# Kernel tuning notes

Hardware: AMD Instinct MI355X
Metric: run time of the kernel (lower is better)

Reference implementation:

```python
import jax, jax.numpy as jnp
import numpy as np

N = 50000        # nodes
E = 1_600_000    # edges (avg degree 32)
G = 512          # graphs
F_IN = 9         # node features
H = 64           # hidden dim
ED = 1           # edge feature dim


def _lin(k, fo, fi):
    w = jax.random.normal(k, (fo, fi), jnp.float32) * (1.0 / np.sqrt(fi))
    b = jnp.zeros((fo,), jnp.float32)
    return w, b


def setup_inputs() -> dict:
    key = jax.random.key(0)
    ks = jax.random.split(key, 16)
    x = jax.random.normal(ks[0], (N, F_IN), jnp.float32)
    edge_index = jax.random.randint(ks[1], (2, E), 0, N, dtype=jnp.int64)
    edge_attr = jax.random.normal(ks[2], (E, ED), jnp.float32)
    batch = jnp.sort(jax.random.randint(ks[3], (N,), 0, G, dtype=jnp.int64))
    B_total = jax.random.uniform(ks[4], (G,), jnp.float32) * 100.0
    terminal_mask = jax.random.randint(ks[5], (N,), 0, 2, dtype=jnp.int32)
    c_cost = jax.random.uniform(ks[6], (N,), jnp.float32)
    # conv1: edge lin (ED->F_IN), nn = Linear(F_IN,H), Linear(H,H)
    e1_w, e1_b = _lin(ks[7], F_IN, ED)
    w1a, b1a = _lin(ks[8], H, F_IN)
    w1b, b1b = _lin(ks[9], H, H)
    # conv2: edge lin (ED->H), nn = Linear(H,H), Linear(H,H)
    e2_w, e2_b = _lin(ks[10], H, ED)
    w2a, b2a = _lin(ks[11], H, H)
    w2b, b2b = _lin(ks[12], H, H)
    # readout: Linear(H,H//2), Linear(H//2,1)
    wr1, br1 = _lin(ks[13], H // 2, H)
    wr2, br2 = _lin(ks[14], 1, H // 2)
    return dict(x=x, edge_index=edge_index, edge_attr=edge_attr, batch=batch,
                B_total=B_total, terminal_mask=terminal_mask, c_cost=c_cost,
                e1_w=e1_w, e1_b=e1_b, w1a=w1a, b1a=b1a, w1b=w1b, b1b=b1b,
                e2_w=e2_w, e2_b=e2_b, w2a=w2a, b2a=b2a, w2b=w2b, b2b=b2b,
                wr1=wr1, br1=br1, wr2=wr2, br2=br2)


def _gine(x, src, dst, edge_attr, ew, eb, wa, ba, wb, bb):
    # GINEConv (eps=0): nn(x + sum_j relu(x_j + W_e e_ji))
    e = edge_attr @ ew.T + eb                    # [E, F]
    m = jax.nn.relu(x[src] + e)                  # [E, F] gather + edge fuse
    aggr = jax.ops.segment_sum(m, dst, num_segments=N)  # scatter-add -> [N, F]
    h = x + aggr
    h = jax.nn.relu(h @ wa.T + ba)
    h = jax.nn.relu(h @ wb.T + bb)
    return h


def reference(x, edge_index, edge_attr, batch, B_total, terminal_mask, c_cost,
              e1_w, e1_b, w1a, b1a, w1b, b1b,
              e2_w, e2_b, w2a, b2a, w2b, b2b,
              wr1, br1, wr2, br2):
    src, dst = edge_index[0], edge_index[1]
    h = _gine(x, src, dst, edge_attr, e1_w, e1_b, w1a, b1a, w1b, b1b)
    h = _gine(h, src, dst, edge_attr, e2_w, e2_b, w2a, b2a, w2b, b2b)
    pi_raw = jax.nn.sigmoid((jax.nn.relu(h @ wr1.T + br1) @ wr2.T + br2))[:, 0]
    pi_raw = pi_raw * (1.0 - terminal_mask.astype(jnp.float32))
    node_expenses = pi_raw * c_cost
    total_expenses = jax.ops.segment_sum(node_expenses, batch, num_segments=G)
    ratio = jnp.minimum(B_total[batch] / (total_expenses[batch] + 1e-12), 1.0)
    return pi_raw * ratio
```

## Files before the change

### kernel.cpp

```cpp
#include <hip/hip_runtime.h>
#include <hip/hip_fp16.h>
#include <math.h>

#define N_NODES 50000
#define N_EDGES 1600000
#define N_GRAPHS 512
#define F_IN 9
#define H 64
#define N_BUCKETS ((N_NODES + 255) >> 8)
#define EPB 4096
#define N_SBLK ((N_EDGES + EPB - 1) / EPB)
#define FINE_CAP 10240

typedef _Float16 f16x8 __attribute__((ext_vector_type(8)));
typedef float f32x4 __attribute__((ext_vector_type(4)));

__device__ __forceinline__ void pack_weights_body(
        const float* __restrict__ w1a, const float* __restrict__ w1b,
        const float* __restrict__ w2a, const float* __restrict__ w2b,
        const float* __restrict__ wr1,
        __half* __restrict__ pk1Ah, __half* __restrict__ pk1Al,
        __half* __restrict__ pk1Bh, __half* __restrict__ pk1Bl,
        __half* __restrict__ pkAh, __half* __restrict__ pkAl,
        __half* __restrict__ pkBh, __half* __restrict__ pkBl,
        __half* __restrict__ pkRh, __half* __restrict__ pkRl) {
    int t = threadIdx.x;
    for (int i = t; i < 2048; i += 512) {
        int j = i & 7, l = (i >> 3) & 63, tt = i >> 9;
        int q = l >> 4, n = l & 15;
        int k = q * 8 + j;
        float v = (k < F_IN) ? w1a[(tt * 16 + n) * F_IN + k] : 0.f;
        __half h = __float2half(v);
        pk1Ah[i] = h; pk1Al[i] = __float2half(v - __half2float(h));
    }
    for (int i = t; i < 4096; i += 512) {
        int j = i & 7, l = (i >> 3) & 63, c = (i >> 9) & 1, tt = i >> 10;
        int q = l >> 4, n = l & 15;
        int src = (tt * 16 + n) * H + c * 32 + q * 8 + j;
        float v1 = w1b[src], wa = w2a[src], wb = w2b[src];
        __half h1 = __float2half(v1), ah = __float2half(wa), bh = __float2half(wb);
        pk1Bh[i] = h1; pk1Bl[i] = __float2half(v1 - __half2float(h1));
        pkAh[i] = ah; pkAl[i] = __float2half(wa - __half2float(ah));
        pkBh[i] = bh; pkBl[i] = __float2half(wb - __half2float(bh));
    }
    for (int i = t; i < 2048; i += 512) {
        int j = i & 7, l = (i >> 3) & 63, c = (i >> 9) & 1, tt = i >> 10;
        int q = l >> 4, n = l & 15;
        float wr = wr1[(tt * 16 + n) * H + c * 32 + q * 8 + j];
        __half rh = __float2half(wr);
        pkRh[i] = rh; pkRl[i] = __float2half(wr - __half2float(rh));
    }
}

__global__ void __launch_bounds__(512)
bucket_scatter(const int* __restrict__ ei,
               const float* __restrict__ ea,
               int* __restrict__ bnext,
               uint2* __restrict__ ebuk,
               const float* __restrict__ w1a,
               const float* __restrict__ w1b,
               const float* __restrict__ w2a,
               const float* __restrict__ w2b,
               const float* __restrict__ wr1,
               __half* pk1Ah, __half* pk1Al,
               __half* pk1Bh, __half* pk1Bl,
               __half* pkAh, __half* pkAl,
               __half* pkBh, __half* pkBl,
               __half* pkRh, __half* pkRl) {
    if (blockIdx.x == 0) {
        pack_weights_body(w1a, w1b, w2a, w2b, wr1, pk1Ah, pk1Al, pk1Bh, pk1Bl,
                          pkAh, pkAl, pkBh, pkBl, pkRh, pkRl);
        return;
    }
    __shared__ int cnt[N_BUCKETS];
    __shared__ int gbase[N_BUCKETS];
    for (int i = threadIdx.x; i < N_BUCKETS; i += 512) cnt[i] = 0;
    __syncthreads();
    int base = (blockIdx.x - 1) * EPB;
    int rk[8];
#pragma unroll
    for (int j = 0; j < 8; ++j) {
        int e = base + j * 512 + threadIdx.x;
        rk[j] = -1;
        if (e < N_EDGES) {
            int d = ei[N_EDGES + e];
            int b = d >> 8;
            int r = atomicAdd(&cnt[b], 1);
            rk[j] = (b << 21) | ((d & 255) << 13) | r;
        }
    }
    __syncthreads();
    for (int i = threadIdx.x; i < N_BUCKETS; i += 512)
        gbase[i] = cnt[i] ? atomicAdd(&bnext[i], cnt[i]) : 0;
    __syncthreads();
#pragma unroll
    for (int j = 0; j < 8; ++j) {
        if (rk[j] < 0) continue;
        int e = base + j * 512 + threadIdx.x;
        int b = rk[j] >> 21, dl = (rk[j] >> 13) & 255, r = rk[j] & 8191;
        int slot = gbase[b] + r;
        if (slot >= FINE_CAP) continue;
        unsigned pay = ((unsigned)ei[e] << 16) |
                       (unsigned)__half_as_ushort(__float2half(ea[e]));
        ebuk[(size_t)b * FINE_CAP + slot] = make_uint2(pay, (unsigned)dl);
    }
}

__global__ void __launch_bounds__(512)
bucket_fine(const uint2* __restrict__ ebuk,
            const int* __restrict__ bnext,
            unsigned* __restrict__ ep4,
            int* __restrict__ starts, int* __restrict__ deg) {
    __shared__ unsigned sorted[FINE_CAP];
    __shared__ int cntN[256], offN[256], nxtN[256];
    __shared__ int wsum[4];
    int b = blockIdx.x;
    int base = b * FINE_CAP;
    int count = bnext[b];
    if (count > FINE_CAP) count = FINE_CAP;
    int tid = threadIdx.x;
    if (tid < 256) cntN[tid] = 0;
    __syncthreads();
    for (int i = tid; i < count; i += 512)
        atomicAdd(&cntN[ebuk[base + i].y], 1);
    __syncthreads();
    int lane = tid & 63, wid = tid >> 6;
    int v = 0, incl = 0;
    if (tid < 256) {
        v = cntN[tid]; incl = v;
#pragma unroll
        for (int off = 1; off < 64; off <<= 1) {
            int t = __shfl_up(incl, off, 64);
            if (lane >= off) incl += t;
        }
        if (lane == 63) wsum[wid] = incl;
    }
    __syncthreads();
    if (tid < 256) {
        int woff = 0;
        for (int w = 0; w < wid; ++w) woff += wsum[w];
        int excl = woff + incl - v;
        offN[tid] = excl;
        nxtN[tid] = 0;
        int n = (b << 8) + tid;
        if (n < N_NODES) { starts[n] = base + excl; deg[n] = v; }
    }
    __syncthreads();
    for (int i = tid; i < count; i += 512) {
        uint2 e = ebuk[base + i];
        int r = atomicAdd(&nxtN[e.y], 1);
        sorted[offN[e.y] + r] = e.x;
    }
    __syncthreads();
    for (int i = tid; i < count; i += 512)
        ep4[base + i] = sorted[i];
}

#define UNPACK_ATTR(P) __half2float(__ushort_as_half((unsigned short)((P) & 0xffffu)))

__global__ void agg1_kernel(const float* __restrict__ x,
                            const int* __restrict__ starts,
                            const int* __restrict__ deg,
                            const unsigned* __restrict__ ep4,
                            const float* __restrict__ e1w,
                            const float* __restrict__ e1b,
                            float* __restrict__ xs) {
    int n = blockIdx.x * (blockDim.x >> 6) + (threadIdx.x >> 6);
    int lane = threadIdx.x & 63;
    if (n >= N_NODES) return;
    int slot = lane >> 4;
    int f = lane & 15;
    int s0 = starts[n], dg = deg[n];
    bool act = f < F_IN;
    float wf = act ? e1w[f] : 0.f;
    float bf = act ? e1b[f] : 0.f;
    float acc = 0.f;
    int j = slot;
    for (; j + 12 < dg; j += 16) {
        unsigned pa = ep4[s0 + j];
        unsigned pb = ep4[s0 + j + 4];
        unsigned pc = ep4[s0 + j + 8];
        unsigned pd = ep4[s0 + j + 12];
        float xa_ = act ? x[(pa >> 16) * F_IN + f] : 0.f;
        float xb_ = act ? x[(pb >> 16) * F_IN + f] : 0.f;
        float xc_ = act ? x[(pc >> 16) * F_IN + f] : 0.f;
        float xd_ = act ? x[(pd >> 16) * F_IN + f] : 0.f;
        if (act) {
            acc += fmaxf(xa_ + UNPACK_ATTR(pa) * wf + bf, 0.f)
                 + fmaxf(xb_ + UNPACK_ATTR(pb) * wf + bf, 0.f)
                 + fmaxf(xc_ + UNPACK_ATTR(pc) * wf + bf, 0.f)
                 + fmaxf(xd_ + UNPACK_ATTR(pd) * wf + bf, 0.f);
        }
    }
    for (; j < dg; j += 4) {
        unsigned p = ep4[s0 + j];
        float xv = act ? x[(p >> 16) * F_IN + f] : 0.f;
        float m = xv + UNPACK_ATTR(p) * wf + bf;
        acc += act ? fmaxf(m, 0.f) : 0.f;
    }
    acc += __shfl_xor(acc, 16, 64);
    acc += __shfl_xor(acc, 32, 64);
    if (lane < 32)
        xs[n * 32 + lane] = (lane < F_IN) ? x[n * F_IN + lane] + acc : 0.f;
}

__device__ __forceinline__ void split8(const float* __restrict__ v,
                                       f16x8& hi, f16x8& lo) {
#pragma unroll
    for (int j = 0; j < 8; ++j) {
        _Float16 h = (_Float16)v[j];
        hi[j] = h;
        lo[j] = (_Float16)(v[j] - (float)h);
    }
}

#define TILE3(C, A0H, A0L, A1H, A1L, PH, PL, T) do {                          \
        f16x8 b0h = *(const f16x8*)((PH) + (((T) * 2 + 0) * 64 + lane) * 8);  \
        f16x8 b0l = *(const f16x8*)((PL) + (((T) * 2 + 0) * 64 + lane) * 8);  \
        f16x8 b1h = *(const f16x8*)((PH) + (((T) * 2 + 1) * 64 + lane) * 8);  \
        f16x8 b1l = *(const f16x8*)((PL) + (((T) * 2 + 1) * 64 + lane) * 8);  \
        C = __builtin_amdgcn_mfma_f32_16x16x32_f16(A0H, b0h, C, 0, 0, 0);     \
        C = __builtin_amdgcn_mfma_f32_16x16x32_f16(A0L, b0h, C, 0, 0, 0);     \
        C = __builtin_amdgcn_mfma_f32_16x16x32_f16(A0H, b0l, C, 0, 0, 0);     \
        C = __builtin_amdgcn_mfma_f32_16x16x32_f16(A1H, b1h, C, 0, 0, 0);     \
        C = __builtin_amdgcn_mfma_f32_16x16x32_f16(A1L, b1h, C, 0, 0, 0);     \
        C = __builtin_amdgcn_mfma_f32_16x16x32_f16(A1H, b1l, C, 0, 0, 0);     \
    } while (0)

__global__ void node1_kernel(const float* __restrict__ xs,
                             const __half* __restrict__ pk1Ah, const __half* __restrict__ pk1Al,
                             const float* __restrict__ b1a,
                             const __half* __restrict__ pk1Bh, const __half* __restrict__ pk1Bl,
                             const float* __restrict__ b1b,
                             __half* __restrict__ h1) {
    __shared__ float hbuf[4][16][68];
    int wv = threadIdx.x >> 6;
    int lane = threadIdx.x & 63;
    int gwave = blockIdx.x * 4 + wv;
    bool active = gwave < (N_NODES / 16);
    int base = active ? gwave * 16 : 0;
    int m = lane & 15, q = lane >> 4;
    const _Float16* pAh = (const _Float16*)pk1Ah;
    const _Float16* pAl = (const _Float16*)pk1Al;
    const _Float16* pBh = (const _Float16*)pk1Bh;
    const _Float16* pBl = (const _Float16*)pk1Bl;

    f16x8 ah, al;
    split8(xs + (size_t)(base + m) * 32 + q * 8, ah, al);
#pragma unroll
    for (int t = 0; t < 4; ++t) {
        f32x4 c = {0.f, 0.f, 0.f, 0.f};
        f16x8 bh = *(const f16x8*)(pAh + (t * 64 + lane) * 8);
        f16x8 bl = *(const f16x8*)(pAl + (t * 64 + lane) * 8);
        c = __builtin_amdgcn_mfma_f32_16x16x32_f16(ah, bh, c, 0, 0, 0);
        c = __builtin_amdgcn_mfma_f32_16x16x32_f16(al, bh, c, 0, 0, 0);
        c = __builtin_amdgcn_mfma_f32_16x16x32_f16(ah, bl, c, 0, 0, 0);
        float bias = b1a[t * 16 + m];
#pragma unroll
        for (int r = 0; r < 4; ++r)
            hbuf[wv][q * 4 + r][t * 16 + m] = fmaxf(c[r] + bias, 0.f);
    }
    __syncthreads();
    f16x8 a0h, a0l, a1h, a1l;
    split8(&hbuf[wv][m][q * 8], a0h, a0l);
    split8(&hbuf[wv][m][32 + q * 8], a1h, a1l);
    float tmp[4][4];
#pragma unroll
    for (int t = 0; t < 4; ++t) {
        f32x4 c = {0.f, 0.f, 0.f, 0.f};
        TILE3(c, a0h, a0l, a1h, a1l, pBh, pBl, t);
        float bias = b1b[t * 16 + m];
#pragma unroll
        for (int r = 0; r < 4; ++r)
            tmp[t][r] = fmaxf(c[r] + bias, 0.f);
    }
    __syncthreads();
#pragma unroll
    for (int t = 0; t < 4; ++t)
#pragma unroll
        for (int r = 0; r < 4; ++r)
            hbuf[wv][q * 4 + r][t * 16 + m] = tmp[t][r];
    __syncthreads();
    if (active) {
        int nn = lane >> 2, part = lane & 3;
        f16x8 vlo, vhi;
        const float* rlo = &hbuf[wv][nn][part * 8];
        const float* rhi = &hbuf[wv][nn][32 + part * 8];
#pragma unroll
        for (int j = 0; j < 8; ++j) {
            vlo[j] = (_Float16)rlo[j];
            vhi[j] = (_Float16)rhi[j];
        }
        *(f16x8*)(h1 + (size_t)(base + nn) * 64 + part * 8) = vlo;
        *(f16x8*)(h1 + (size_t)(base + nn) * 64 + 32 + part * 8) = vhi;
    }
}

__global__ void aggphase2_kernel(const __half* __restrict__ h1,
                                 const int* __restrict__ starts,
                                 const int* __restrict__ deg,
                                 const unsigned* __restrict__ ep4,
                                 const float* __restrict__ ew,
                                 const float* __restrict__ eb,
                                 float* __restrict__ htot) {
    int n = blockIdx.x * (blockDim.x >> 6) + (threadIdx.x >> 6);
    int lane = threadIdx.x & 63;
    if (n >= N_NODES) return;
    int s0 = starts[n], dg = deg[n];
    const unsigned* ep = ep4 + s0;
    float wf = ew[lane], bf = eb[lane];
    float acc = 0.f;
#define EDGE1(P, V) acc += fmaxf((V) + UNPACK_ATTR(P) * wf + bf, 0.f)
    int j = 0;
    for (; j + 8 <= dg; j += 8) {
        unsigned p0 = ep[j + 0], p1 = ep[j + 1], p2 = ep[j + 2], p3 = ep[j + 3];
        unsigned p4 = ep[j + 4], p5 = ep[j + 5], p6 = ep[j + 6], p7 = ep[j + 7];
        float v0 = __half2float(h1[(size_t)(p0 >> 16) * 64 + lane]);
        float v1 = __half2float(h1[(size_t)(p1 >> 16) * 64 + lane]);
        float v2 = __half2float(h1[(size_t)(p2 >> 16) * 64 + lane]);
        float v3 = __half2float(h1[(size_t)(p3 >> 16) * 64 + lane]);
        float v4 = __half2float(h1[(size_t)(p4 >> 16) * 64 + lane]);
        float v5 = __half2float(h1[(size_t)(p5 >> 16) * 64 + lane]);
        float v6 = __half2float(h1[(size_t)(p6 >> 16) * 64 + lane]);
        float v7 = __half2float(h1[(size_t)(p7 >> 16) * 64 + lane]);
        EDGE1(p0, v0); EDGE1(p1, v1); EDGE1(p2, v2); EDGE1(p3, v3);
        EDGE1(p4, v4); EDGE1(p5, v5); EDGE1(p6, v6); EDGE1(p7, v7);
    }
    if (j + 4 <= dg) {
        unsigned p0 = ep[j + 0], p1 = ep[j + 1], p2 = ep[j + 2], p3 = ep[j + 3];
        float v0 = __half2float(h1[(size_t)(p0 >> 16) * 64 + lane]);
        float v1 = __half2float(h1[(size_t)(p1 >> 16) * 64 + lane]);
        float v2 = __half2float(h1[(size_t)(p2 >> 16) * 64 + lane]);
        float v3 = __half2float(h1[(size_t)(p3 >> 16) * 64 + lane]);
        EDGE1(p0, v0); EDGE1(p1, v1); EDGE1(p2, v2); EDGE1(p3, v3);
        j += 4;
    }
    for (; j < dg; ++j) {
        unsigned p = ep[j];
        float v = __half2float(h1[(size_t)(p >> 16) * 64 + lane]);
        EDGE1(p, v);
    }
#undef EDGE1
    float self = __half2float(h1[(size_t)n * 64 + lane]);
    htot[(size_t)n * 64 + lane] = self + acc;
}

__global__ void node2_kernel(const float* __restrict__ htot,
                             const __half* __restrict__ pkAh, const __half* __restrict__ pkAl,
                             const float* __restrict__ b2a,
                             const __half* __restrict__ pkBh, const __half* __restrict__ pkBl,
                             const float* __restrict__ b2b,
                             const __half* __restrict__ pkRh, const __half* __restrict__ pkRl,
                             const float* __restrict__ br1,
                             const float* __restrict__ wr2,
                             const float* __restrict__ br2,
                             const int* __restrict__ term,
                             const int* __restrict__ batch,
                             const float* __restrict__ ccost,
                             float* __restrict__ pi,
                             float* __restrict__ te) {
    __shared__ float hbuf[4][16][68];
    int wv = threadIdx.x >> 6;
    int lane = threadIdx.x & 63;
    int gwave = blockIdx.x * 4 + wv;
    bool active = gwave < (N_NODES / 16);
    int base = active ? gwave * 16 : 0;
    int m = lane & 15, q = lane >> 4;
    const _Float16* pAh = (const _Float16*)pkAh;
    const _Float16* pAl = (const _Float16*)pkAl;
    const _Float16* pBh = (const _Float16*)pkBh;
    const _Float16* pBl = (const _Float16*)pkBl;
    const _Float16* pRh = (const _Float16*)pkRh;
    const _Float16* pRl = (const _Float16*)pkRl;

    f16x8 a0h, a0l, a1h, a1l;
    {
        const float* hrow = htot + (size_t)(base + m) * 64;
        split8(hrow + q * 8, a0h, a0l);
        split8(hrow + 32 + q * 8, a1h, a1l);
    }
#pragma unroll
    for (int t = 0; t < 4; ++t) {
        f32x4 c = {0.f, 0.f, 0.f, 0.f};
        TILE3(c, a0h, a0l, a1h, a1l, pAh, pAl, t);
        float bias = b2a[t * 16 + m];
#pragma unroll
        for (int r = 0; r < 4; ++r)
            hbuf[wv][q * 4 + r][t * 16 + m] = fmaxf(c[r] + bias, 0.f);
    }
    __syncthreads();
    split8(&hbuf[wv][m][q * 8], a0h, a0l);
    split8(&hbuf[wv][m][32 + q * 8], a1h, a1l);
    float tmp[4][4];
#pragma unroll
    for (int t = 0; t < 4; ++t) {
        f32x4 c = {0.f, 0.f, 0.f, 0.f};
        TILE3(c, a0h, a0l, a1h, a1l, pBh, pBl, t);
        float bias = b2b[t * 16 + m];
#pragma unroll
        for (int r = 0; r < 4; ++r)
            tmp[t][r] = fmaxf(c[r] + bias, 0.f);
    }
    __syncthreads();
#pragma unroll
    for (int t = 0; t < 4; ++t)
#pragma unroll
        for (int r = 0; r < 4; ++r)
            hbuf[wv][q * 4 + r][t * 16 + m] = tmp[t][r];
    __syncthreads();
    split8(&hbuf[wv][m][q * 8], a0h, a0l);
    split8(&hbuf[wv][m][32 + q * 8], a1h, a1l);
    float partial[4] = {0.f, 0.f, 0.f, 0.f};
#pragma unroll
    for (int t = 0; t < 2; ++t) {
        f32x4 c = {0.f, 0.f, 0.f, 0.f};
        TILE3(c, a0h, a0l, a1h, a1l, pRh, pRl, t);
        float bias = br1[t * 16 + m];
        float wv2 = wr2[t * 16 + m];
#pragma unroll
        for (int r = 0; r < 4; ++r)
            partial[r] += fmaxf(c[r] + bias, 0.f) * wv2;
    }
#pragma unroll
    for (int off = 1; off < 16; off <<= 1) {
        partial[0] += __shfl_xor(partial[0], off, 64);
        partial[1] += __shfl_xor(partial[1], off, 64);
        partial[2] += __shfl_xor(partial[2], off, 64);
        partial[3] += __shfl_xor(partial[3], off, 64);
    }
    if (active && m == 0) {
#pragma unroll
        for (int r = 0; r < 4; ++r) {
            int n = base + q * 4 + r;
            float z = partial[r] + br2[0];
            float sig = 1.f / (1.f + expf(-z));
            float pv = sig * (1.f - (float)term[n]);
            pi[n] = pv;
            float contrib = pv * ccost[n];
            if (contrib != 0.f) atomicAdd(&te[batch[n]], contrib);
        }
    }
}

__global__ void final_kernel(const float* __restrict__ pi,
                             const int* __restrict__ batch,
                             const float* __restrict__ Btot,
                             const float* __restrict__ te,
                             float* __restrict__ out) {
    int n = blockIdx.x * blockDim.x + threadIdx.x;
    if (n >= N_NODES) return;
    int b = batch[n];
    float ratio = fminf(Btot[b] / (te[b] + 1e-12f), 1.f);
    out[n] = pi[n] * ratio;
}

extern "C" void kernel_launch(void* const* d_in, const int* in_sizes, int n_in,
                              void* d_out, int out_size, void* d_ws, size_t ws_size,
                              hipStream_t stream) {
    const float* x     = (const float*)d_in[0];
    const int*   ei    = (const int*)d_in[1];
    const float* ea    = (const float*)d_in[2];
    const int*   batch = (const int*)d_in[3];
    const float* Btot  = (const float*)d_in[4];
    const int*   term  = (const int*)d_in[5];
    const float* ccost = (const float*)d_in[6];
    const float* e1w   = (const float*)d_in[7];
    const float* e1b   = (const float*)d_in[8];
    const float* w1a   = (const float*)d_in[9];
    const float* b1a   = (const float*)d_in[10];
    const float* w1b   = (const float*)d_in[11];
    const float* b1b   = (const float*)d_in[12];
    const float* e2w   = (const float*)d_in[13];
    const float* e2b   = (const float*)d_in[14];
    const float* w2a   = (const float*)d_in[15];
    const float* b2a   = (const float*)d_in[16];
    const float* w2b   = (const float*)d_in[17];
    const float* b2b   = (const float*)d_in[18];
    const float* wr1   = (const float*)d_in[19];
    const float* br1   = (const float*)d_in[20];
    const float* wr2   = (const float*)d_in[21];
    const float* br2   = (const float*)d_in[22];

    char* p = (char*)d_ws;
    int*      bnext  = (int*)p;      p += sizeof(int)      * 256;
    float*    te     = (float*)p;    p += sizeof(float)    * N_GRAPHS;
    int*      starts = (int*)p;      p += sizeof(int)      * N_NODES;
    int*      deg    = (int*)p;      p += sizeof(int)      * N_NODES;
    p = (char*)(((size_t)p + 15) & ~(size_t)15);
    uint2*    ebuk   = (uint2*)p;    p += sizeof(uint2)    * (size_t)N_BUCKETS * FINE_CAP;
    unsigned* ep4    = (unsigned*)p; p += sizeof(unsigned) * (size_t)N_BUCKETS * FINE_CAP;
    __half*   h1     = (__half*)p;   p += sizeof(__half)   * (size_t)N_NODES * 64;
    float*    htot   = (float*)p;    p += sizeof(float)    * (size_t)N_NODES * 64;
    float*    xs     = (float*)p;    p += sizeof(float)    * (size_t)N_NODES * 32;
    float*    pi     = (float*)p;    p += sizeof(float)    * N_NODES;
    __half*   pk1Ah  = (__half*)p;   p += sizeof(__half)   * 2048;
    __half*   pk1Al  = (__half*)p;   p += sizeof(__half)   * 2048;
    __half*   pk1Bh  = (__half*)p;   p += sizeof(__half)   * 4096;
    __half*   pk1Bl  = (__half*)p;   p += sizeof(__half)   * 4096;
    __half*   pkAh   = (__half*)p;   p += sizeof(__half)   * 4096;
    __half*   pkAl   = (__half*)p;   p += sizeof(__half)   * 4096;
    __half*   pkBh   = (__half*)p;   p += sizeof(__half)   * 4096;
    __half*   pkBl   = (__half*)p;   p += sizeof(__half)   * 4096;
    __half*   pkRh   = (__half*)p;   p += sizeof(__half)   * 2048;
    __half*   pkRl   = (__half*)p;   p += sizeof(__half)   * 2048;
    float*    out    = (float*)d_out;

    hipMemsetAsync(d_ws, 0, sizeof(int) * 256 + sizeof(float) * N_GRAPHS, stream);

    bucket_scatter<<<1 + N_SBLK, 512, 0, stream>>>(ei, ea, bnext, ebuk,
                                                   w1a, w1b, w2a, w2b, wr1,
                                                   pk1Ah, pk1Al, pk1Bh, pk1Bl,
                                                   pkAh, pkAl, pkBh, pkBl, pkRh, pkRl);
    bucket_fine<<<N_BUCKETS, 512, 0, stream>>>(ebuk, bnext, ep4, starts, deg);
    agg1_kernel<<<(N_NODES + 3) / 4, 256, 0, stream>>>(x, starts, deg, ep4, e1w, e1b, xs);
    node1_kernel<<<(N_NODES / 16 + 3) / 4, 256, 0, stream>>>(xs, pk1Ah, pk1Al, b1a,
                                                             pk1Bh, pk1Bl, b1b, h1);
    aggphase2_kernel<<<(N_NODES + 3) / 4, 256, 0, stream>>>(h1, starts, deg, ep4,
                                                            e2w, e2b, htot);
    node2_kernel<<<(N_NODES / 16 + 3) / 4, 256, 0, stream>>>(htot,
                                                             pkAh, pkAl, b2a,
                                                             pkBh, pkBl, b2b,
                                                             pkRh, pkRl, br1,
                                                             wr2, br2, term,
                                                             batch, ccost, pi, te);
    final_kernel<<<(N_NODES + 255) / 256, 256, 0, stream>>>(pi, batch, Btot, te, out);
}
```

Measured before the change: 245.8 us.

## Split layer-2 aggregation feature halves across XCDs and keep bucket edges in registers

The layer-2 aggregation kernel now launches twice as many blocks. Block IDs are mapped so that each group of four XCDs handles one 32-feature half of h1. Within a wave, the two 32-lane halves take alternating edges and are combined with a shuffle. The aim is to shrink the h1 working set seen by each XCD's L2, at the cost of extra edge-index reads and idle lanes on the final store. Separately, bucket_scatter now loads src and attr in its first pass, and bucket_fine keeps up to 20 edges per thread in registers so ebuk is read once instead of twice. The 20-entry register array adds register pressure.

```diff
diff --git a/kernel.cpp b/kernel.cpp
--- a/kernel.cpp
+++ b/kernel.cpp
@@ -78,12 +78,17 @@
     __syncthreads();
     int base = (blockIdx.x - 1) * EPB;
     int rk[8];
+    unsigned pay[8];
 #pragma unroll
     for (int j = 0; j < 8; ++j) {
         int e = base + j * 512 + threadIdx.x;
         rk[j] = -1;
         if (e < N_EDGES) {
             int d = ei[N_EDGES + e];
+            int s = ei[e];
+            float a = ea[e];
+            pay[j] = ((unsigned)s << 16) |
+                     (unsigned)__half_as_ushort(__float2half(a));
             int b = d >> 8;
             int r = atomicAdd(&cnt[b], 1);
             rk[j] = (b << 21) | ((d & 255) << 13) | r;
@@ -96,13 +101,10 @@
 #pragma unroll
     for (int j = 0; j < 8; ++j) {
         if (rk[j] < 0) continue;
-        int e = base + j * 512 + threadIdx.x;
         int b = rk[j] >> 21, dl = (rk[j] >> 13) & 255, r = rk[j] & 8191;
         int slot = gbase[b] + r;
         if (slot >= FINE_CAP) continue;
-        unsigned pay = ((unsigned)ei[e] << 16) |
-                       (unsigned)__half_as_ushort(__float2half(ea[e]));
-        ebuk[(size_t)b * FINE_CAP + slot] = make_uint2(pay, (unsigned)dl);
+        ebuk[(size_t)b * FINE_CAP + slot] = make_uint2(pay[j], (unsigned)dl);
     }
 }
 
@@ -121,8 +123,15 @@
     int tid = threadIdx.x;
     if (tid < 256) cntN[tid] = 0;
     __syncthreads();
-    for (int i = tid; i < count; i += 512)
-        atomicAdd(&cntN[ebuk[base + i].y], 1);
+    uint2 ev[20];
+#pragma unroll
+    for (int k = 0; k < 20; ++k) {
+        int i = tid + k * 512;
+        ev[k] = (i < count) ? ebuk[base + i] : make_uint2(0u, 0xFFFFFFFFu);
+    }
+#pragma unroll
+    for (int k = 0; k < 20; ++k)
+        if (ev[k].y < 256u) atomicAdd(&cntN[ev[k].y], 1);
     __syncthreads();
     int lane = tid & 63, wid = tid >> 6;
     int v = 0, incl = 0;
@@ -146,10 +155,12 @@
         if (n < N_NODES) { starts[n] = base + excl; deg[n] = v; }
     }
     __syncthreads();
-    for (int i = tid; i < count; i += 512) {
-        uint2 e = ebuk[base + i];
-        int r = atomicAdd(&nxtN[e.y], 1);
-        sorted[offN[e.y] + r] = e.x;
+#pragma unroll
+    for (int k = 0; k < 20; ++k) {
+        if (ev[k].y < 256u) {
+            int r = atomicAdd(&nxtN[ev[k].y], 1);
+            sorted[offN[ev[k].y] + r] = ev[k].x;
+        }
     }
     __syncthreads();
     for (int i = tid; i < count; i += 512)
@@ -303,46 +314,54 @@
                                  const float* __restrict__ ew,
                                  const float* __restrict__ eb,
                                  float* __restrict__ htot) {
-    int n = blockIdx.x * (blockDim.x >> 6) + (threadIdx.x >> 6);
+    int xcd = blockIdx.x & 7;
+    int hoff = (xcd >> 2) * 32;
+    int grp = (blockIdx.x >> 3) * 4 + (xcd & 3);
+    int wv = threadIdx.x >> 6;
+    int n = grp * 4 + wv;
     int lane = threadIdx.x & 63;
     if (n >= N_NODES) return;
+    int par = lane >> 5;
+    int fh = lane & 31;
+    int f = hoff + fh;
     int s0 = starts[n], dg = deg[n];
     const unsigned* ep = ep4 + s0;
-    float wf = ew[lane], bf = eb[lane];
+    float wf = ew[f], bf = eb[f];
     float acc = 0.f;
 #define EDGE1(P, V) acc += fmaxf((V) + UNPACK_ATTR(P) * wf + bf, 0.f)
     int j = 0;
-    for (; j + 8 <= dg; j += 8) {
-        unsigned p0 = ep[j + 0], p1 = ep[j + 1], p2 = ep[j + 2], p3 = ep[j + 3];
-        unsigned p4 = ep[j + 4], p5 = ep[j + 5], p6 = ep[j + 6], p7 = ep[j + 7];
-        float v0 = __half2float(h1[(size_t)(p0 >> 16) * 64 + lane]);
-        float v1 = __half2float(h1[(size_t)(p1 >> 16) * 64 + lane]);
-        float v2 = __half2float(h1[(size_t)(p2 >> 16) * 64 + lane]);
-        float v3 = __half2float(h1[(size_t)(p3 >> 16) * 64 + lane]);
-        float v4 = __half2float(h1[(size_t)(p4 >> 16) * 64 + lane]);
-        float v5 = __half2float(h1[(size_t)(p5 >> 16) * 64 + lane]);
-        float v6 = __half2float(h1[(size_t)(p6 >> 16) * 64 + lane]);
-        float v7 = __half2float(h1[(size_t)(p7 >> 16) * 64 + lane]);
+    for (; j + 16 <= dg; j += 16) {
+        unsigned p0 = ep[j +  0 + par], p1 = ep[j +  2 + par];
+        unsigned p2 = ep[j +  4 + par], p3 = ep[j +  6 + par];
+        unsigned p4 = ep[j +  8 + par], p5 = ep[j + 10 + par];
+        unsigned p6 = ep[j + 12 + par], p7 = ep[j + 14 + par];
+        float v0 = __half2float(h1[(size_t)(p0 >> 16) * 64 + f]);
+        float v1 = __half2float(h1[(size_t)(p1 >> 16) * 64 + f]);
+        float v2 = __half2float(h1[(size_t)(p2 >> 16) * 64 + f]);
+        float v3 = __half2float(h1[(size_t)(p3 >> 16) * 64 + f]);
+        float v4 = __half2float(h1[(size_t)(p4 >> 16) * 64 + f]);
+        float v5 = __half2float(h1[(size_t)(p5 >> 16) * 64 + f]);
+        float v6 = __half2float(h1[(size_t)(p6 >> 16) * 64 + f]);
+        float v7 = __half2float(h1[(size_t)(p7 >> 16) * 64 + f]);
         EDGE1(p0, v0); EDGE1(p1, v1); EDGE1(p2, v2); EDGE1(p3, v3);
         EDGE1(p4, v4); EDGE1(p5, v5); EDGE1(p6, v6); EDGE1(p7, v7);
     }
-    if (j + 4 <= dg) {
-        unsigned p0 = ep[j + 0], p1 = ep[j + 1], p2 = ep[j + 2], p3 = ep[j + 3];
-        float v0 = __half2float(h1[(size_t)(p0 >> 16) * 64 + lane]);
-        float v1 = __half2float(h1[(size_t)(p1 >> 16) * 64 + lane]);
-        float v2 = __half2float(h1[(size_t)(p2 >> 16) * 64 + lane]);
-        float v3 = __half2float(h1[(size_t)(p3 >> 16) * 64 + lane]);
-        EDGE1(p0, v0); EDGE1(p1, v1); EDGE1(p2, v2); EDGE1(p3, v3);
-        j += 4;
-    }
-    for (; j < dg; ++j) {
+    for (; j + 2 <= dg; j += 2) {
+        unsigned p = ep[j + par];
+        float v = __half2float(h1[(size_t)(p >> 16) * 64 + f]);
+        EDGE1(p, v);
+    }
+    if (j < dg && par == 0) {
         unsigned p = ep[j];
-        float v = __half2float(h1[(size_t)(p >> 16) * 64 + lane]);
+        float v = __half2float(h1[(size_t)(p >> 16) * 64 + f]);
         EDGE1(p, v);
     }
 #undef EDGE1
-    float self = __half2float(h1[(size_t)n * 64 + lane]);
-    htot[(size_t)n * 64 + lane] = self + acc;
+    acc += __shfl_xor(acc, 32, 64);
+    if (par == 0) {
+        float self = __half2float(h1[(size_t)n * 64 + f]);
+        htot[(size_t)n * 64 + f] = self + acc;
+    }
 }
 
 __global__ void node2_kernel(const float* __restrict__ htot,
@@ -515,8 +534,8 @@
     agg1_kernel<<<(N_NODES + 3) / 4, 256, 0, stream>>>(x, starts, deg, ep4, e1w, e1b, xs);
     node1_kernel<<<(N_NODES / 16 + 3) / 4, 256, 0, stream>>>(xs, pk1Ah, pk1Al, b1a,
                                                              pk1Bh, pk1Bl, b1b, h1);
-    aggphase2_kernel<<<(N_NODES + 3) / 4, 256, 0, stream>>>(h1, starts, deg, ep4,
-                                                            e2w, e2b, htot);
+    aggphase2_kernel<<<25000, 256, 0, stream>>>(h1, starts, deg, ep4,
+                                                e2w, e2b, htot);
     node2_kernel<<<(N_NODES / 16 + 3) / 4, 256, 0, stream>>>(htot,
                                                              pkAh, pkAl, b2a,
                                                              pkBh, pkBl, b2b,
```

Measured after the change: 265.3 us. 1.08x slower.

## Cache edge payloads in registers during bucketing and use nontemporal loads/stores

Applied to the files above, without the earlier changes.

The coarse bucketing pass now loads source index and edge attribute alongside the destination in its first loop and keeps the packed payload in registers, so it no longer re-reads them after the global offset step. The fine bucketing kernel loads its bucket entries once into a 20-element register array and reuses them for both the histogram and the scatter, instead of reading global memory twice. The aggregation kernels switch edge-list reads and output writes to nontemporal loads and stores to reduce cache pollution. The register arrays raise register pressure and can lower occupancy. Nontemporal hints on the packed edge list may also be harmful, because ep4 is read by both aggregation passes and again by lanes within the same wave.

```diff
diff --git a/kernel.cpp b/kernel.cpp
--- a/kernel.cpp
+++ b/kernel.cpp
@@ -78,12 +78,17 @@
     __syncthreads();
     int base = (blockIdx.x - 1) * EPB;
     int rk[8];
+    unsigned pay[8];
 #pragma unroll
     for (int j = 0; j < 8; ++j) {
         int e = base + j * 512 + threadIdx.x;
         rk[j] = -1;
         if (e < N_EDGES) {
             int d = ei[N_EDGES + e];
+            int s = ei[e];
+            float a = ea[e];
+            pay[j] = ((unsigned)s << 16) |
+                     (unsigned)__half_as_ushort(__float2half(a));
             int b = d >> 8;
             int r = atomicAdd(&cnt[b], 1);
             rk[j] = (b << 21) | ((d & 255) << 13) | r;
@@ -96,13 +101,10 @@
 #pragma unroll
     for (int j = 0; j < 8; ++j) {
         if (rk[j] < 0) continue;
-        int e = base + j * 512 + threadIdx.x;
         int b = rk[j] >> 21, dl = (rk[j] >> 13) & 255, r = rk[j] & 8191;
         int slot = gbase[b] + r;
         if (slot >= FINE_CAP) continue;
-        unsigned pay = ((unsigned)ei[e] << 16) |
-                       (unsigned)__half_as_ushort(__float2half(ea[e]));
-        ebuk[(size_t)b * FINE_CAP + slot] = make_uint2(pay, (unsigned)dl);
+        ebuk[(size_t)b * FINE_CAP + slot] = make_uint2(pay[j], (unsigned)dl);
     }
 }
 
@@ -121,8 +123,15 @@
     int tid = threadIdx.x;
     if (tid < 256) cntN[tid] = 0;
     __syncthreads();
-    for (int i = tid; i < count; i += 512)
-        atomicAdd(&cntN[ebuk[base + i].y], 1);
+    uint2 ev[20];
+#pragma unroll
+    for (int k = 0; k < 20; ++k) {
+        int i = tid + k * 512;
+        ev[k] = (i < count) ? ebuk[base + i] : make_uint2(0u, 0xFFFFFFFFu);
+    }
+#pragma unroll
+    for (int k = 0; k < 20; ++k)
+        if (ev[k].y < 256u) atomicAdd(&cntN[ev[k].y], 1);
     __syncthreads();
     int lane = tid & 63, wid = tid >> 6;
     int v = 0, incl = 0;
@@ -146,10 +155,12 @@
         if (n < N_NODES) { starts[n] = base + excl; deg[n] = v; }
     }
     __syncthreads();
-    for (int i = tid; i < count; i += 512) {
-        uint2 e = ebuk[base + i];
-        int r = atomicAdd(&nxtN[e.y], 1);
-        sorted[offN[e.y] + r] = e.x;
+#pragma unroll
+    for (int k = 0; k < 20; ++k) {
+        if (ev[k].y < 256u) {
+            int r = atomicAdd(&nxtN[ev[k].y], 1);
+            sorted[offN[ev[k].y] + r] = ev[k].x;
+        }
     }
     __syncthreads();
     for (int i = tid; i < count; i += 512)
@@ -177,10 +188,10 @@
     float acc = 0.f;
     int j = slot;
     for (; j + 12 < dg; j += 16) {
-        unsigned pa = ep4[s0 + j];
-        unsigned pb = ep4[s0 + j + 4];
-        unsigned pc = ep4[s0 + j + 8];
-        unsigned pd = ep4[s0 + j + 12];
+        unsigned pa = __builtin_nontemporal_load(ep4 + s0 + j);
+        unsigned pb = __builtin_nontemporal_load(ep4 + s0 + j + 4);
+        unsigned pc = __builtin_nontemporal_load(ep4 + s0 + j + 8);
+        unsigned pd = __builtin_nontemporal_load(ep4 + s0 + j + 12);
         float xa_ = act ? x[(pa >> 16) * F_IN + f] : 0.f;
         float xb_ = act ? x[(pb >> 16) * F_IN + f] : 0.f;
         float xc_ = act ? x[(pc >> 16) * F_IN + f] : 0.f;
@@ -193,15 +204,17 @@
         }
     }
     for (; j < dg; j += 4) {
-        unsigned p = ep4[s0 + j];
+        unsigned p = __builtin_nontemporal_load(ep4 + s0 + j);
         float xv = act ? x[(p >> 16) * F_IN + f] : 0.f;
         float m = xv + UNPACK_ATTR(p) * wf + bf;
         acc += act ? fmaxf(m, 0.f) : 0.f;
     }
     acc += __shfl_xor(acc, 16, 64);
     acc += __shfl_xor(acc, 32, 64);
-    if (lane < 32)
-        xs[n * 32 + lane] = (lane < F_IN) ? x[n * F_IN + lane] + acc : 0.f;
+    if (lane < 32) {
+        float v = (lane < F_IN) ? x[n * F_IN + lane] + acc : 0.f;
+        __builtin_nontemporal_store(v, xs + n * 32 + lane);
+    }
 }
 
 __device__ __forceinline__ void split8(const float* __restrict__ v,
@@ -313,8 +326,14 @@
 #define EDGE1(P, V) acc += fmaxf((V) + UNPACK_ATTR(P) * wf + bf, 0.f)
     int j = 0;
     for (; j + 8 <= dg; j += 8) {
-        unsigned p0 = ep[j + 0], p1 = ep[j + 1], p2 = ep[j + 2], p3 = ep[j + 3];
-        unsigned p4 = ep[j + 4], p5 = ep[j + 5], p6 = ep[j + 6], p7 = ep[j + 7];
+        unsigned p0 = __builtin_nontemporal_load(ep + j + 0);
+        unsigned p1 = __builtin_nontemporal_load(ep + j + 1);
+        unsigned p2 = __builtin_nontemporal_load(ep + j + 2);
+        unsigned p3 = __builtin_nontemporal_load(ep + j + 3);
+        unsigned p4 = __builtin_nontemporal_load(ep + j + 4);
+        unsigned p5 = __builtin_nontemporal_load(ep + j + 5);
+        unsigned p6 = __builtin_nontemporal_load(ep + j + 6);
+        unsigned p7 = __builtin_nontemporal_load(ep + j + 7);
         float v0 = __half2float(h1[(size_t)(p0 >> 16) * 64 + lane]);
         float v1 = __half2float(h1[(size_t)(p1 >> 16) * 64 + lane]);
         float v2 = __half2float(h1[(size_t)(p2 >> 16) * 64 + lane]);
@@ -327,7 +346,10 @@
         EDGE1(p4, v4); EDGE1(p5, v5); EDGE1(p6, v6); EDGE1(p7, v7);
     }
     if (j + 4 <= dg) {
-        unsigned p0 = ep[j + 0], p1 = ep[j + 1], p2 = ep[j + 2], p3 = ep[j + 3];
+        unsigned p0 = __builtin_nontemporal_load(ep + j + 0);
+        unsigned p1 = __builtin_nontemporal_load(ep + j + 1);
+        unsigned p2 = __builtin_nontemporal_load(ep + j + 2);
+        unsigned p3 = __builtin_nontemporal_load(ep + j + 3);
         float v0 = __half2float(h1[(size_t)(p0 >> 16) * 64 + lane]);
         float v1 = __half2float(h1[(size_t)(p1 >> 16) * 64 + lane]);
         float v2 = __half2float(h1[(size_t)(p2 >> 16) * 64 + lane]);
@@ -336,13 +358,13 @@
         j += 4;
     }
     for (; j < dg; ++j) {
-        unsigned p = ep[j];
+        unsigned p = __builtin_nontemporal_load(ep + j);
         float v = __half2float(h1[(size_t)(p >> 16) * 64 + lane]);
         EDGE1(p, v);
     }
 #undef EDGE1
     float self = __half2float(h1[(size_t)n * 64 + lane]);
-    htot[(size_t)n * 64 + lane] = self + acc;
+    __builtin_nontemporal_store(self + acc, htot + (size_t)n * 64 + lane);
 }
 
 __global__ void node2_kernel(const float* __restrict__ htot,
```

Measured after the change: 252.4 us. +2.7%, slower.
